# Kernel optimization log

Hardware: AMD Instinct MI355X
Metric: run time of the kernel (lower is better)

## Reference

```python
import jax, jax.numpy as jnp
import numpy as np

B, SEQ, EMB, LAT = 8192, 1024, 768, 256
TAXA = ['phylum', 'order', 'family', 'genus', 'species']
NC = {'phylum': 40, 'order': 200, 'family': 800, 'genus': 3000, 'species': 12000}


def _table(P, C):
    # parent->child validity: child c belongs to parent (c % P); every parent non-empty
    return (jnp.arange(C)[None, :] % P) == jnp.arange(P)[:, None]


def setup_inputs() -> dict:
    key = jax.random.key(0)
    ks = jax.random.split(key, 16)
    d = {}
    d['sequences'] = jax.random.normal(ks[0], (B, SEQ), jnp.float32)
    d['W_dnabert'] = jax.random.normal(ks[1], (SEQ, EMB), jnp.float32) * 0.02
    d['W_enc'] = jax.random.normal(ks[2], (EMB, LAT), jnp.float32) * 0.02
    for i, t in enumerate(TAXA):
        d[f'W_cls_{t}'] = jax.random.normal(ks[3 + i], (LAT, NC[t]), jnp.float32) * 0.02
        d[f'W_dec_{t}'] = jax.random.normal(ks[8 + i], (LAT, EMB), jnp.float32) * 0.02
    d['W_global'] = jax.random.normal(ks[13], (LAT, EMB), jnp.float32) * 0.02
    d['T_order'] = _table(NC['phylum'], NC['order'])
    d['T_family'] = _table(NC['order'], NC['family'])
    d['T_genus'] = _table(NC['family'], NC['genus'])
    d['T_species'] = _table(NC['genus'], NC['species'])
    return d


def reference(sequences, W_dnabert, W_enc,
              W_cls_phylum, W_cls_order, W_cls_family, W_cls_genus, W_cls_species,
              W_dec_phylum, W_dec_order, W_dec_family, W_dec_genus, W_dec_species,
              W_global, T_order, T_family, T_genus, T_species):
    # frozen dnabert (torch.no_grad)
    emb = jax.lax.stop_gradient(sequences @ W_dnabert)          # [B, EMB]
    z = emb @ W_enc                                             # [B, LAT]

    Wc = {'phylum': W_cls_phylum, 'order': W_cls_order, 'family': W_cls_family,
          'genus': W_cls_genus, 'species': W_cls_species}
    Wd = {'phylum': W_dec_phylum, 'order': W_dec_order, 'family': W_dec_family,
          'genus': W_dec_genus, 'species': W_dec_species}
    Tt = {'order': T_order, 'family': T_family, 'genus': T_genus, 'species': T_species}

    logits_out, recon_out = {}, {}
    parent_preds = None
    for taxon in TAXA:
        logits = z @ Wc[taxon]                                  # [B, C_taxon]
        if parent_preds is not None and taxon in Tt:
            # vectorized hierarchical mask: gather valid-class row per sample
            mask = Tt[taxon][parent_preds]                      # [B, C_taxon] bool
            logits = jnp.where(mask, logits, -jnp.inf)
        logits_out[taxon] = logits
        recon_out[taxon] = z @ Wd[taxon]                        # [B, EMB]
        parent_preds = jnp.argmax(logits, axis=1)               # [B] int

    global_rec = z @ W_global                                   # [B, EMB]
    return (z,
            logits_out['phylum'], logits_out['order'], logits_out['family'],
            logits_out['genus'], logits_out['species'],
            recon_out['phylum'], recon_out['order'], recon_out['family'],
            recon_out['genus'], recon_out['species'],
            global_rec, emb)
```

## Files before the change

kernel.cpp:

```cpp
#include <hip/hip_runtime.h>
#include <hip/hip_bf16.h>

typedef __attribute__((ext_vector_type(8))) short short8;
typedef __attribute__((ext_vector_type(4))) float f32x4;
typedef unsigned short ushort_t;
typedef unsigned int u32;

static constexpr int Bn  = 8192;
static constexpr int SEQ = 1024;
static constexpr int EMB = 768;
static constexpr int LAT = 256;

static constexpr size_t OFF_Z   = 0;
static constexpr size_t OFF_LP  = 2097152;
static constexpr size_t OFF_LO  = 2424832;
static constexpr size_t OFF_LF  = 4063232;
static constexpr size_t OFF_LG  = 10616832;
static constexpr size_t OFF_LS  = 35192832;
static constexpr size_t OFF_RP  = 133496832;
static constexpr size_t OFF_EMB = 171245568;

static constexpr size_t SCR      = OFF_LO;
static constexpr size_t S_SEQ_H  = SCR + 0;
static constexpr size_t S_SEQ_L  = SCR + 4194304;
static constexpr size_t S_EMB_H  = SCR + 8388608;
static constexpr size_t S_EMB_L  = SCR + 11534336;
static constexpr size_t S_Z_H    = SCR + 14680064;
static constexpr size_t S_Z_L    = SCR + 15728640;
static constexpr size_t S_REC_H  = SCR + 16777216;
static constexpr size_t S_REC_L  = SCR + 17367040;
static constexpr size_t S_CLS_T  = SCR + 17956864;
static constexpr size_t S_T_O    = S_CLS_T + 0;
static constexpr size_t S_T_F    = S_CLS_T + 51200;
static constexpr size_t S_T_G    = S_CLS_T + 256000;
static constexpr size_t S_T_S    = S_CLS_T + 1024000;

static constexpr size_t SCR_END   = SCR + 22052864;
static constexpr size_t TAIL_N4   = (OFF_RP - SCR_END) / 4;
static constexpr size_t T_SEQ0 = 0,        T_SEQ1 = 3276800;
static constexpr size_t T_EMB0 = 3276800,  T_EMB1 = 16384000;
static constexpr size_t T_Z0   = 16384000, T_Z1   = 18743296;
static constexpr size_t T_R0   = 18743296, T_R1   = 27254784;
static constexpr size_t FILLZ_N4  = 8388608 / 4;
static constexpr size_t FILLR_N4  = (14680064 - 8388608) / 4;
static constexpr size_t FILLB_N4  = (22052864 - 14680064) / 4;

static constexpr size_t WS_DNA_H = 0;
static constexpr size_t WS_DNA_L = 786432;
static constexpr size_t WS_ENC_H = 1572864;
static constexpr size_t WS_ENC_L = 1769472;
static constexpr size_t WS_COMPACT_FL = 983040;

#define MASKED_VAL (-1.0e30f)

__device__ __forceinline__ ushort_t bfbits(float f) {
    return __builtin_bit_cast(ushort_t, __float2bfloat16(f));
}
__device__ __forceinline__ float bf2f(ushort_t h) {
    return __builtin_bit_cast(float, ((unsigned)h) << 16);
}
__device__ __forceinline__ void split2(float f, ushort_t& h, ushort_t& l) {
    h = bfbits(f);
    l = bfbits(f - bf2f(h));
}

__device__ __forceinline__ size_t tile_pos(int rt, int nKT, int kt, int r, int g) {
    return ((size_t)rt * nKT + kt) * 8192 + (size_t)r * 64 + ((g ^ (r & 7)) << 3);
}

__device__ __forceinline__ void fill_span(f32x4* __restrict__ dst, size_t n4,
                                          int fb, int nFB)
{
    const f32x4 v = {MASKED_VAL, MASKED_VAL, MASKED_VAL, MASKED_VAL};
    for (size_t i = (size_t)fb * 256 + threadIdx.x; i < n4; i += (size_t)nFB * 256)
        __builtin_nontemporal_store(v, dst + i);
}

__global__ __launch_bounds__(256)
void fill_kernel(f32x4* __restrict__ dst, size_t n4)
{
    fill_span(dst, n4, blockIdx.x, gridDim.x);
}

__device__ __forceinline__ void prep_wtT_body(const float* __restrict__ src,
                                              ushort_t* __restrict__ dh,
                                              ushort_t* __restrict__ dl,
                                              int K, int N, int bx, int nb)
{
    const int gpr = K >> 3, nKT = K >> 6;
    const int nG = N * gpr;
    for (int gi = bx * 256 + threadIdx.x; gi < nG; gi += nb * 256) {
        const int n = gi / gpr, gk = gi - n * gpr;
        short8 hh, ll;
        #pragma unroll
        for (int j = 0; j < 8; ++j) {
            ushort_t hv, lv;
            split2(src[(size_t)(gk * 8 + j) * N + n], hv, lv);
            hh[j] = (short)hv; ll[j] = (short)lv;
        }
        const size_t base = tile_pos(n >> 7, nKT, gk >> 3, n & 127, gk & 7);
        *(short8*)(dh + base) = hh;
        *(short8*)(dl + base) = ll;
    }
}

struct Ptr6 { const float* p[6]; };

__device__ __forceinline__ void prep_rec_body(Ptr6 s, ushort_t* __restrict__ dh,
                                              ushort_t* __restrict__ dl, int bx, int nb)
{
    constexpr int gpr = 32, nKT = 4;
    const int nG = 4608 * gpr;
    for (int gi = bx * 256 + threadIdx.x; gi < nG; gi += nb * 256) {
        const int np = gi / gpr, gk = gi - np * gpr;
        const int m = np / 768, nn = np - m * 768;
        const float* sm = s.p[m];
        short8 hh, ll;
        #pragma unroll
        for (int j = 0; j < 8; ++j) {
            ushort_t hv, lv;
            split2(sm[(size_t)(gk * 8 + j) * 768 + nn], hv, lv);
            hh[j] = (short)hv; ll[j] = (short)lv;
        }
        const size_t base = tile_pos(np >> 7, nKT, gk >> 3, np & 127, gk & 7);
        *(short8*)(dh + base) = hh;
        *(short8*)(dl + base) = ll;
    }
}

__global__ __launch_bounds__(256)
void prep_all(const float* __restrict__ Wdna, ushort_t* dnaH, ushort_t* dnaL,
              const float* __restrict__ Wenc, ushort_t* encH, ushort_t* encL,
              Ptr6 s6, ushort_t* recH, ushort_t* recL)
{
    const int bx = blockIdx.x;
    if (bx < 384)       prep_wtT_body(Wdna, dnaH, dnaL, 1024, 768, bx, 384);
    else if (bx < 480)  prep_wtT_body(Wenc, encH, encL, 768, 256, bx - 384, 96);
    else                prep_rec_body(s6, recH, recL, bx - 480, 576);
}

__global__ __launch_bounds__(256)
void transpose_all(const float* __restrict__ Wo, const float* __restrict__ Wf,
                   const float* __restrict__ Wg, const float* __restrict__ Ws,
                   float* To, float* Tf, float* Tg, float* Ts)
{
    __shared__ float t[64][65];
    int bx = blockIdx.x;
    const float* src; float* dst; int C; int cb;
    if (bx < 16)       { src = Wo; dst = To; C = 200;   cb = bx; }
    else if (bx < 68)  { src = Wf; dst = Tf; C = 800;   cb = bx - 16; }
    else if (bx < 256) { src = Wg; dst = Tg; C = 3000;  cb = bx - 68; }
    else               { src = Ws; dst = Ts; C = 12000; cb = bx - 256; }
    const int ct = cb >> 2, kt = cb & 3;
    const int c0 = ct * 64;
    const int tid = threadIdx.x;
    const int cl = tid & 63, kr = tid >> 6;
    #pragma unroll
    for (int i = 0; i < 16; ++i) {
        const int k = i * 4 + kr;
        const int c = c0 + cl;
        t[k][cl] = (c < C) ? src[(size_t)(kt * 64 + k) * C + c] : 0.f;
    }
    __syncthreads();
    #pragma unroll
    for (int i = 0; i < 16; ++i) {
        const int cc = i * 4 + kr;
        const int c = c0 + cc;
        if (c < C) dst[(size_t)c * 256 + kt * 64 + cl] = t[cl][cc];
    }
}

__global__ __launch_bounds__(256)
void split_tiled_fill(const float* __restrict__ src, ushort_t* __restrict__ dh,
                      ushort_t* __restrict__ dl, int M, int K,
                      int nGB, f32x4* __restrict__ f1, size_t n1)
{
    if ((int)blockIdx.x >= nGB) {
        fill_span(f1, n1, blockIdx.x - nGB, gridDim.x - nGB);
        return;
    }
    const int gpr = K >> 3, nKT = K >> 6;
    const int nG = M * gpr;
    for (int gi = blockIdx.x * 256 + threadIdx.x; gi < nG; gi += nGB * 256) {
        const int row = gi / gpr, gk = gi - row * gpr;
        const float* s = src + (size_t)row * K + gk * 8;
        const float4 a = *(const float4*)s;
        const float4 b = *(const float4*)(s + 4);
        const float f[8] = {a.x, a.y, a.z, a.w, b.x, b.y, b.z, b.w};
        short8 hh, ll;
        #pragma unroll
        for (int j = 0; j < 8; ++j) {
            ushort_t hv, lv;
            split2(f[j], hv, lv);
            hh[j] = (short)hv; ll[j] = (short)lv;
        }
        const size_t base = tile_pos(row >> 7, nKT, gk >> 3, row & 127, gk & 7);
        *(short8*)(dh + base) = hh;
        *(short8*)(dl + base) = ll;
    }
}

__global__ __launch_bounds__(256)
void split_tiled(const float* __restrict__ src, ushort_t* __restrict__ dh,
                 ushort_t* __restrict__ dl, int M, int K)
{
    const int gpr = K >> 3, nKT = K >> 6;
    const int nG = M * gpr;
    for (int gi = blockIdx.x * 256 + threadIdx.x; gi < nG; gi += gridDim.x * 256) {
        const int row = gi / gpr, gk = gi - row * gpr;
        const float* s = src + (size_t)row * K + gk * 8;
        const float4 a = *(const float4*)s;
        const float4 b = *(const float4*)(s + 4);
        const float f[8] = {a.x, a.y, a.z, a.w, b.x, b.y, b.z, b.w};
        short8 hh, ll;
        #pragma unroll
        for (int j = 0; j < 8; ++j) {
            ushort_t hv, lv;
            split2(f[j], hv, lv);
            hh[j] = (short)hv; ll[j] = (short)lv;
        }
        const size_t base = tile_pos(row >> 7, nKT, gk >> 3, row & 127, gk & 7);
        *(short8*)(dh + base) = hh;
        *(short8*)(dl + base) = ll;
    }
}

__device__ __forceinline__ void gload16(const ushort_t* g, ushort_t* l) {
    __builtin_amdgcn_global_load_lds(
        (const __attribute__((address_space(1))) u32*)g,
        (__attribute__((address_space(3))) u32*)l, 16, 0, 0);
}

__global__ __launch_bounds__(256)
void gemm_ts_fill(const ushort_t* __restrict__ Ahg, const ushort_t* __restrict__ Alg,
                  const ushort_t* __restrict__ Bhg, const ushort_t* __restrict__ Blg,
                  int K, float* __restrict__ Cbase, int chunkW, size_t chunkStride,
                  int nCT, int nGB,
                  f32x4* __restrict__ f1, size_t n1,
                  f32x4* __restrict__ f2, size_t n2)
{
    __shared__ ushort_t sAh[8192], sAl[8192], sBh[8192], sBl[8192];

    if ((int)blockIdx.x >= nGB) {
        const int fb = blockIdx.x - nGB, nFB = gridDim.x - nGB;
        fill_span(f1, n1, fb, nFB);
        if (n2) fill_span(f2, n2, fb, nFB);
        return;
    }

    const int tid = threadIdx.x, w = tid >> 6, lane = tid & 63;
    const int wm = w >> 1, wn = w & 1;
    const int fr = lane & 15, kg = lane >> 4;
    const int nKT = K >> 6;
    const int rt = blockIdx.x / nCT, ct = blockIdx.x % nCT;
    const int col0 = ct * 128;
    const int chunk = col0 / chunkW;
    const int lc0 = col0 - chunk * chunkW;
    float* __restrict__ C = Cbase + (size_t)chunk * chunkStride;

    const int sbase = w * 2048;
    const int lgo = lane * 8;

    f32x4 acc[4][4] = {};

    for (int kt = 0; kt < nKT; ++kt) {
        const size_t at = ((size_t)rt * nKT + kt) * 8192;
        const size_t bt = ((size_t)ct * nKT + kt) * 8192;
        #pragma unroll
        for (int i = 0; i < 4; ++i) {
            const int co = sbase + i * 512;
            gload16(Ahg + at + co + lgo, &sAh[co]);
            gload16(Alg + at + co + lgo, &sAl[co]);
            gload16(Bhg + bt + co + lgo, &sBh[co]);
            gload16(Blg + bt + co + lgo, &sBl[co]);
        }
        __syncthreads();

        #pragma unroll
        for (int ks = 0; ks < 2; ++ks) {
            const int g = ks * 4 + kg;
            short8 a_h[4], a_l[4], b_h[4], b_l[4];
            #pragma unroll
            for (int i = 0; i < 4; ++i) {
                const int ra = wm * 64 + i * 16 + fr;
                const int pa = ra * 64 + ((g ^ (ra & 7)) << 3);
                a_h[i] = *(const short8*)&sAh[pa];
                a_l[i] = *(const short8*)&sAl[pa];
                const int rb = wn * 64 + i * 16 + fr;
                const int pb = rb * 64 + ((g ^ (rb & 7)) << 3);
                b_h[i] = *(const short8*)&sBh[pb];
                b_l[i] = *(const short8*)&sBl[pb];
            }
            #pragma unroll
            for (int mi = 0; mi < 4; ++mi) {
                #pragma unroll
                for (int ni = 0; ni < 4; ++ni) {
                    acc[mi][ni] = __builtin_amdgcn_mfma_f32_16x16x32_bf16(a_h[mi], b_h[ni], acc[mi][ni], 0, 0, 0);
                    acc[mi][ni] = __builtin_amdgcn_mfma_f32_16x16x32_bf16(a_h[mi], b_l[ni], acc[mi][ni], 0, 0, 0);
                    acc[mi][ni] = __builtin_amdgcn_mfma_f32_16x16x32_bf16(a_l[mi], b_h[ni], acc[mi][ni], 0, 0, 0);
                }
            }
        }
        __syncthreads();
    }

    const int crow = kg * 4;
    #pragma unroll
    for (int mi = 0; mi < 4; ++mi) {
        const int gr = rt * 128 + wm * 64 + mi * 16 + crow;
        #pragma unroll
        for (int ni = 0; ni < 4; ++ni) {
            const int gc = lc0 + wn * 64 + ni * 16 + fr;
            #pragma unroll
            for (int j = 0; j < 4; ++j)
                C[(size_t)(gr + j) * chunkW + gc] = acc[mi][ni][j];
        }
    }
}

template <int C, int P>
__device__ __forceinline__ int level_w(const float* __restrict__ WT,
                                       float4 zr, int p, int lane,
                                       float* __restrict__ rec )
{
    const int cnt = (C - p + P - 1) / P;
    float sv[5];
    #pragma unroll
    for (int j = 0; j < 5; ++j) {
        float s = 0.f;
        if (j < cnt) {
            const float4 wv = *(const float4*)(WT + (size_t)(p + j * P) * 256 + lane * 4);
            s = fmaf(wv.x, zr.x, fmaf(wv.y, zr.y, fmaf(wv.z, zr.z, wv.w * zr.w)));
        }
        sv[j] = s;
    }
    #pragma unroll
    for (int j = 0; j < 5; ++j) {
        if (j < cnt) {
            #pragma unroll
            for (int off = 32; off; off >>= 1) sv[j] += __shfl_xor(sv[j], off);
        }
    }
    float best = sv[0];
    int bj = 0;
    #pragma unroll
    for (int j = 1; j < 5; ++j)
        if (j < cnt && sv[j] > best) { best = sv[j]; bj = j; }

    if (lane == 0) {
        rec[0] = __int_as_float(p);
        rec[1] = sv[0];
        rec[2] = (1 < cnt) ? sv[1] : 0.f;
        rec[3] = (2 < cnt) ? sv[2] : 0.f;
        rec[4] = (3 < cnt) ? sv[3] : 0.f;
        rec[5] = (4 < cnt) ? sv[4] : 0.f;
    }
    return p + bj * P;
}

__global__ __launch_bounds__(256)
void chain_kernel(const float* __restrict__ z,
                  const float* __restrict__ Wp,
                  const float* __restrict__ ToT, const float* __restrict__ TfT,
                  const float* __restrict__ TgT, const float* __restrict__ TsT,
                  float* __restrict__ out, float* __restrict__ compact)
{
    __shared__ float zsh[4][256];

    const int w    = threadIdx.x >> 6;
    const int lane = threadIdx.x & 63;
    const size_t b = (size_t)blockIdx.x * 4 + w;

    const float4 zr4 = *(const float4*)(z + b * 256 + lane * 4);
    *(float4*)&zsh[w][lane * 4] = zr4;
    asm volatile("s_waitcnt lgkmcnt(0)" ::: "memory");
    const float* zrow = &zsh[w][0];

    float pv = MASKED_VAL;
    if (lane < 40) {
        float s0 = 0.f, s1 = 0.f, s2 = 0.f, s3 = 0.f;
        #pragma unroll 4
        for (int k = 0; k < 256; k += 4) {
            s0 = fmaf(zrow[k + 0], Wp[(k + 0) * 40 + lane], s0);
            s1 = fmaf(zrow[k + 1], Wp[(k + 1) * 40 + lane], s1);
            s2 = fmaf(zrow[k + 2], Wp[(k + 2) * 40 + lane], s2);
            s3 = fmaf(zrow[k + 3], Wp[(k + 3) * 40 + lane], s3);
        }
        pv = (s0 + s1) + (s2 + s3);
        out[OFF_LP + b * 40 + lane] = pv;
    }
    float v = pv;
    int idx = lane;
    #pragma unroll
    for (int off = 32; off; off >>= 1) {
        float ov = __shfl_xor(v, off);
        int   oi = __shfl_xor(idx, off);
        if (ov > v || (ov == v && oi < idx)) { v = ov; idx = oi; }
    }
    int p = idx;

    p = level_w<200, 40>    (ToT, zr4, p, lane, compact + (0 * Bn + b) * 6);
    p = level_w<800, 200>   (TfT, zr4, p, lane, compact + (1 * Bn + b) * 6);
    p = level_w<3000, 800>  (TgT, zr4, p, lane, compact + (2 * Bn + b) * 6);
    (void)level_w<12000, 3000>(TsT, zr4, p, lane, compact + (3 * Bn + b) * 6);
}

__global__ __launch_bounds__(256)
void scatter_kernel(const float* __restrict__ compact, float* __restrict__ out)
{
    const int t = blockIdx.x * 256 + threadIdx.x;
    if (t >= 4 * Bn) return;
    const int lvl = t >> 13, b = t & (Bn - 1);
    const int Cs[4] = {200, 800, 3000, 12000};
    const int Ps[4] = {40, 200, 800, 3000};
    const size_t OFFL[4] = {OFF_LO, OFF_LF, OFF_LG, OFF_LS};
    const float* rec = compact + ((size_t)lvl * Bn + b) * 6;
    const int p = __float_as_int(rec[0]);
    const int C = Cs[lvl], P = Ps[lvl];
    const int cnt = (C - p + P - 1) / P;
    float* dst = out + OFFL[lvl] + (size_t)b * C;
    for (int j = 0; j < cnt; ++j)
        dst[p + j * P] = rec[1 + j];
}

extern "C" void kernel_launch(void* const* d_in, const int* in_sizes, int n_in,
                              void* d_out, int out_size, void* d_ws, size_t ws_size,
                              hipStream_t stream)
{
    const float* seq    = (const float*)d_in[0];
    const float* Wdna   = (const float*)d_in[1];
    const float* Wenc   = (const float*)d_in[2];
    const float* Wcls_p = (const float*)d_in[3];
    const float* Wdec_p = (const float*)d_in[4];
    const float* Wcls_o = (const float*)d_in[5];
    const float* Wdec_o = (const float*)d_in[6];
    const float* Wcls_f = (const float*)d_in[7];
    const float* Wdec_f = (const float*)d_in[8];
    const float* Wcls_g = (const float*)d_in[9];
    const float* Wdec_g = (const float*)d_in[10];
    const float* Wcls_s = (const float*)d_in[11];
    const float* Wdec_s = (const float*)d_in[12];
    const float* Wglob  = (const float*)d_in[13];
    (void)in_sizes; (void)n_in; (void)out_size; (void)ws_size;

    float* out = (float*)d_out;
    ushort_t* ws = (ushort_t*)d_ws;

    ushort_t* seqH = (ushort_t*)(out + S_SEQ_H);
    ushort_t* seqL = (ushort_t*)(out + S_SEQ_L);
    ushort_t* embH = (ushort_t*)(out + S_EMB_H);
    ushort_t* embL = (ushort_t*)(out + S_EMB_L);
    ushort_t* zH   = (ushort_t*)(out + S_Z_H);
    ushort_t* zL   = (ushort_t*)(out + S_Z_L);
    ushort_t* recH = (ushort_t*)(out + S_REC_H);
    ushort_t* recL = (ushort_t*)(out + S_REC_L);
    float* ToT = out + S_T_O;
    float* TfT = out + S_T_F;
    float* TgT = out + S_T_G;
    float* TsT = out + S_T_S;
    ushort_t* dnaH = ws + WS_DNA_H;
    ushort_t* dnaL = ws + WS_DNA_L;
    ushort_t* encH = ws + WS_ENC_H;
    ushort_t* encL = ws + WS_ENC_L;
    float* compact = (float*)ws + WS_COMPACT_FL;
    f32x4* tail = (f32x4*)(out + SCR_END);

    Ptr6 s6{{Wdec_p, Wdec_o, Wdec_f, Wdec_g, Wdec_s, Wglob}};
    prep_all<<<1056, 256, 0, stream>>>(Wdna, dnaH, dnaL, Wenc, encH, encL, s6, recH, recL);
    transpose_all<<<1008, 256, 0, stream>>>(Wcls_o, Wcls_f, Wcls_g, Wcls_s,
                                            ToT, TfT, TgT, TsT);
    split_tiled_fill<<<4096 + 448, 256, 0, stream>>>(seq, seqH, seqL, Bn, SEQ,
                                                     4096, tail + T_SEQ0, T_SEQ1 - T_SEQ0);

    gemm_ts_fill<<<384 + 1664, 256, 0, stream>>>(
        seqH, seqL, dnaH, dnaL, SEQ, out + OFF_EMB, EMB, 0, 6, 384,
        tail + T_EMB0, T_EMB1 - T_EMB0, nullptr, 0);
    split_tiled<<<3072, 256, 0, stream>>>(out + OFF_EMB, embH, embL, Bn, EMB);

    gemm_ts_fill<<<128 + 896, 256, 0, stream>>>(
        embH, embL, encH, encL, EMB, out + OFF_Z, LAT, 0, 2, 128,
        (f32x4*)(out + SCR), FILLZ_N4, tail + T_Z0, T_Z1 - T_Z0);
    split_tiled<<<1024, 256, 0, stream>>>(out + OFF_Z, zH, zL, Bn, LAT);

    gemm_ts_fill<<<2304 + 768, 256, 0, stream>>>(
        zH, zL, recH, recL, LAT, out + OFF_RP, EMB, (size_t)Bn * EMB, 36, 2304,
        (f32x4*)(out + S_EMB_H), FILLR_N4, tail + T_R0, T_R1 - T_R0);

    chain_kernel<<<dim3(Bn / 4), 256, 0, stream>>>(out + OFF_Z, Wcls_p, ToT, TfT,
                                                   TgT, TsT, out, compact);

    fill_kernel<<<512, 256, 0, stream>>>((f32x4*)(out + S_Z_H), FILLB_N4);
    scatter_kernel<<<(4 * Bn + 255) / 256, 256, 0, stream>>>(compact, out);
}
```

Measured before the change: 308.6 us.

## Fuse split into GEMM epilogues and merge prep, recon and chain launches

Each GEMM now stages its result tile through shared memory, writes it with coalesced float4 stores, and also emits the bf16 hi/lo tiled split of the output. This removes the separate split_tiled passes over emb and z. The three prep kernels become one launch, and the recon GEMM, the hierarchical chain and the fills share a single grid, cutting launch count and letting the chain overlap with the GEMM. In exchange the fill spans are rebalanced and the epilogue costs one extra shared-memory round trip and a barrier.

```diff
diff --git a/kernel.cpp b/kernel.cpp
--- a/kernel.cpp
+++ b/kernel.cpp
@@ -37,10 +37,9 @@
 
 static constexpr size_t SCR_END   = SCR + 22052864;
 static constexpr size_t TAIL_N4   = (OFF_RP - SCR_END) / 4;
-static constexpr size_t T_SEQ0 = 0,        T_SEQ1 = 3276800;
-static constexpr size_t T_EMB0 = 3276800,  T_EMB1 = 16384000;
-static constexpr size_t T_Z0   = 16384000, T_Z1   = 18743296;
-static constexpr size_t T_R0   = 18743296, T_R1   = 27254784;
+static constexpr size_t TE0 = 0,        TE1 = 9437184;
+static constexpr size_t TZ0 = 9437184,  TZ1 = 11534336;
+static constexpr size_t TR0 = 11534336, TR1 = 27254784;
 static constexpr size_t FILLZ_N4  = 8388608 / 4;
 static constexpr size_t FILLR_N4  = (14680064 - 8388608) / 4;
 static constexpr size_t FILLB_N4  = (22052864 - 14680064) / 4;
@@ -128,24 +127,11 @@
     }
 }
 
-__global__ __launch_bounds__(256)
-void prep_all(const float* __restrict__ Wdna, ushort_t* dnaH, ushort_t* dnaL,
-              const float* __restrict__ Wenc, ushort_t* encH, ushort_t* encL,
-              Ptr6 s6, ushort_t* recH, ushort_t* recL)
-{
-    const int bx = blockIdx.x;
-    if (bx < 384)       prep_wtT_body(Wdna, dnaH, dnaL, 1024, 768, bx, 384);
-    else if (bx < 480)  prep_wtT_body(Wenc, encH, encL, 768, 256, bx - 384, 96);
-    else                prep_rec_body(s6, recH, recL, bx - 480, 576);
-}
-
-__global__ __launch_bounds__(256)
-void transpose_all(const float* __restrict__ Wo, const float* __restrict__ Wf,
-                   const float* __restrict__ Wg, const float* __restrict__ Ws,
-                   float* To, float* Tf, float* Tg, float* Ts)
-{
-    __shared__ float t[64][65];
-    int bx = blockIdx.x;
+__device__ __forceinline__ void transpose_body(float t[64][65], int bx,
+    const float* __restrict__ Wo, const float* __restrict__ Wf,
+    const float* __restrict__ Wg, const float* __restrict__ Ws,
+    float* To, float* Tf, float* Tg, float* Ts)
+{
     const float* src; float* dst; int C; int cb;
     if (bx < 16)       { src = Wo; dst = To; C = 200;   cb = bx; }
     else if (bx < 68)  { src = Wf; dst = Tf; C = 800;   cb = bx - 16; }
@@ -170,18 +156,14 @@
     }
 }
 
-__global__ __launch_bounds__(256)
-void split_tiled_fill(const float* __restrict__ src, ushort_t* __restrict__ dh,
-                      ushort_t* __restrict__ dl, int M, int K,
-                      int nGB, f32x4* __restrict__ f1, size_t n1)
-{
-    if ((int)blockIdx.x >= nGB) {
-        fill_span(f1, n1, blockIdx.x - nGB, gridDim.x - nGB);
-        return;
-    }
+__device__ __forceinline__ void split_body(const float* __restrict__ src,
+                                           ushort_t* __restrict__ dh,
+                                           ushort_t* __restrict__ dl,
+                                           int M, int K, int bx, int nb)
+{
     const int gpr = K >> 3, nKT = K >> 6;
     const int nG = M * gpr;
-    for (int gi = blockIdx.x * 256 + threadIdx.x; gi < nG; gi += nGB * 256) {
+    for (int gi = bx * 256 + threadIdx.x; gi < nG; gi += nb * 256) {
         const int row = gi / gpr, gk = gi - row * gpr;
         const float* s = src + (size_t)row * K + gk * 8;
         const float4 a = *(const float4*)s;
@@ -201,27 +183,23 @@
 }
 
 __global__ __launch_bounds__(256)
-void split_tiled(const float* __restrict__ src, ushort_t* __restrict__ dh,
-                 ushort_t* __restrict__ dl, int M, int K)
-{
-    const int gpr = K >> 3, nKT = K >> 6;
-    const int nG = M * gpr;
-    for (int gi = blockIdx.x * 256 + threadIdx.x; gi < nG; gi += gridDim.x * 256) {
-        const int row = gi / gpr, gk = gi - row * gpr;
-        const float* s = src + (size_t)row * K + gk * 8;
-        const float4 a = *(const float4*)s;
-        const float4 b = *(const float4*)(s + 4);
-        const float f[8] = {a.x, a.y, a.z, a.w, b.x, b.y, b.z, b.w};
-        short8 hh, ll;
-        #pragma unroll
-        for (int j = 0; j < 8; ++j) {
-            ushort_t hv, lv;
-            split2(f[j], hv, lv);
-            hh[j] = (short)hv; ll[j] = (short)lv;
-        }
-        const size_t base = tile_pos(row >> 7, nKT, gk >> 3, row & 127, gk & 7);
-        *(short8*)(dh + base) = hh;
-        *(short8*)(dl + base) = ll;
+void prep_everything(const float* Wdna, ushort_t* dnaH, ushort_t* dnaL,
+                     const float* Wenc, ushort_t* encH, ushort_t* encL,
+                     Ptr6 s6, ushort_t* recH, ushort_t* recL,
+                     const float* Wo, const float* Wf, const float* Wg, const float* Ws,
+                     float* To, float* Tf, float* Tg, float* Ts,
+                     const float* seq, ushort_t* seqH, ushort_t* seqL)
+{
+    __shared__ float t[64][65];
+    const int bx = blockIdx.x;
+    if (bx < 1056) {
+        if (bx < 384)       prep_wtT_body(Wdna, dnaH, dnaL, 1024, 768, bx, 384);
+        else if (bx < 480)  prep_wtT_body(Wenc, encH, encL, 768, 256, bx - 384, 96);
+        else                prep_rec_body(s6, recH, recL, bx - 480, 576);
+    } else if (bx < 2064) {
+        transpose_body(t, bx - 1056, Wo, Wf, Wg, Ws, To, Tf, Tg, Ts);
+    } else {
+        split_body(seq, seqH, seqL, Bn, SEQ, bx - 2064, 4096);
     }
 }
 
@@ -231,28 +209,23 @@
         (__attribute__((address_space(3))) u32*)l, 16, 0, 0);
 }
 
-__global__ __launch_bounds__(256)
-void gemm_ts_fill(const ushort_t* __restrict__ Ahg, const ushort_t* __restrict__ Alg,
-                  const ushort_t* __restrict__ Bhg, const ushort_t* __restrict__ Blg,
-                  int K, float* __restrict__ Cbase, int chunkW, size_t chunkStride,
-                  int nCT, int nGB,
-                  f32x4* __restrict__ f1, size_t n1,
-                  f32x4* __restrict__ f2, size_t n2)
-{
-    __shared__ ushort_t sAh[8192], sAl[8192], sBh[8192], sBl[8192];
-
-    if ((int)blockIdx.x >= nGB) {
-        const int fb = blockIdx.x - nGB, nFB = gridDim.x - nGB;
-        fill_span(f1, n1, fb, nFB);
-        if (n2) fill_span(f2, n2, fb, nFB);
-        return;
-    }
+__device__ __forceinline__ void gemm_body(
+    ushort_t* smem,
+    const ushort_t* __restrict__ Ahg, const ushort_t* __restrict__ Alg,
+    const ushort_t* __restrict__ Bhg, const ushort_t* __restrict__ Blg,
+    int K, float* __restrict__ Cbase, int chunkW, size_t chunkStride,
+    int nCT, int bx, ushort_t* __restrict__ th, ushort_t* __restrict__ tl, int nKT2)
+{
+    ushort_t* sAh = smem;
+    ushort_t* sAl = smem + 8192;
+    ushort_t* sBh = smem + 16384;
+    ushort_t* sBl = smem + 24576;
 
     const int tid = threadIdx.x, w = tid >> 6, lane = tid & 63;
     const int wm = w >> 1, wn = w & 1;
     const int fr = lane & 15, kg = lane >> 4;
     const int nKT = K >> 6;
-    const int rt = blockIdx.x / nCT, ct = blockIdx.x % nCT;
+    const int rt = bx / nCT, ct = bx % nCT;
     const int col0 = ct * 128;
     const int chunk = col0 / chunkW;
     const int lc0 = col0 - chunk * chunkW;
@@ -304,18 +277,63 @@
         __syncthreads();
     }
 
+    float* cf = (float*)smem;
     const int crow = kg * 4;
     #pragma unroll
-    for (int mi = 0; mi < 4; ++mi) {
-        const int gr = rt * 128 + wm * 64 + mi * 16 + crow;
+    for (int mi = 0; mi < 4; ++mi)
         #pragma unroll
-        for (int ni = 0; ni < 4; ++ni) {
-            const int gc = lc0 + wn * 64 + ni * 16 + fr;
+        for (int ni = 0; ni < 4; ++ni)
             #pragma unroll
             for (int j = 0; j < 4; ++j)
-                C[(size_t)(gr + j) * chunkW + gc] = acc[mi][ni][j];
-        }
-    }
+                cf[(wm * 64 + mi * 16 + crow + j) * 128 + (wn * 64 + ni * 16 + fr)] = acc[mi][ni][j];
+    __syncthreads();
+
+    #pragma unroll
+    for (int i = 0; i < 8; ++i) {
+        const int t = i * 256 + tid;
+        const int row = t >> 4, g = t & 15;
+        const float* srcr = cf + row * 128 + g * 8;
+        const float4 v0 = *(const float4*)srcr;
+        const float4 v1 = *(const float4*)(srcr + 4);
+        float* dst = C + (size_t)(rt * 128 + row) * chunkW + lc0 + g * 8;
+        *(float4*)dst = v0;
+        *(float4*)(dst + 4) = v1;
+        if (th) {
+            const float fv[8] = {v0.x, v0.y, v0.z, v0.w, v1.x, v1.y, v1.z, v1.w};
+            short8 hh, ll;
+            #pragma unroll
+            for (int q = 0; q < 8; ++q) {
+                ushort_t hv, lv;
+                split2(fv[q], hv, lv);
+                hh[q] = (short)hv; ll[q] = (short)lv;
+            }
+            const int ktile = (ct * 128 + g * 8) >> 6;
+            const int gg = g & 7;
+            const size_t base = ((size_t)rt * nKT2 + ktile) * 8192
+                              + (size_t)row * 64 + ((gg ^ (row & 7)) << 3);
+            *(short8*)(th + base) = hh;
+            *(short8*)(tl + base) = ll;
+        }
+    }
+}
+
+__global__ __launch_bounds__(256)
+void gemm_fused(const ushort_t* __restrict__ Ahg, const ushort_t* __restrict__ Alg,
+                const ushort_t* __restrict__ Bhg, const ushort_t* __restrict__ Blg,
+                int K, float* __restrict__ Cbase, int chunkW, size_t chunkStride,
+                int nCT, int nGB, ushort_t* th, ushort_t* tl, int nKT2,
+                f32x4* __restrict__ f1, size_t n1,
+                f32x4* __restrict__ f2, size_t n2)
+{
+    __shared__ ushort_t smem[32768];
+    if ((int)blockIdx.x >= nGB) {
+        const int fb = blockIdx.x - nGB, nFB = gridDim.x - nGB;
+        fill_span(f1, n1, fb, nFB);
+        if (n2) fill_span(f2, n2, fb, nFB);
+        return;
+    }
+    gemm_body(smem, Ahg, Alg, Bhg, Blg, K, Cbase, chunkW, chunkStride,
+              nCT, blockIdx.x, th, tl, nKT2);
 }
 
 template <int C, int P>
@@ -358,23 +376,20 @@
     return p + bj * P;
 }
 
-__global__ __launch_bounds__(256)
-void chain_kernel(const float* __restrict__ z,
-                  const float* __restrict__ Wp,
-                  const float* __restrict__ ToT, const float* __restrict__ TfT,
-                  const float* __restrict__ TgT, const float* __restrict__ TsT,
-                  float* __restrict__ out, float* __restrict__ compact)
-{
-    __shared__ float zsh[4][256];
-
+__device__ __forceinline__ void chain_body(float* zsh, int bid,
+    const float* __restrict__ z, const float* __restrict__ Wp,
+    const float* __restrict__ ToT, const float* __restrict__ TfT,
+    const float* __restrict__ TgT, const float* __restrict__ TsT,
+    float* __restrict__ out, float* __restrict__ compact)
+{
     const int w    = threadIdx.x >> 6;
     const int lane = threadIdx.x & 63;
-    const size_t b = (size_t)blockIdx.x * 4 + w;
+    const size_t b = (size_t)bid * 4 + w;
 
     const float4 zr4 = *(const float4*)(z + b * 256 + lane * 4);
-    *(float4*)&zsh[w][lane * 4] = zr4;
+    *(float4*)&zsh[w * 256 + lane * 4] = zr4;
     asm volatile("s_waitcnt lgkmcnt(0)" ::: "memory");
-    const float* zrow = &zsh[w][0];
+    const float* zrow = zsh + w * 256;
 
     float pv = MASKED_VAL;
     if (lane < 40) {
@@ -403,6 +418,31 @@
     p = level_w<800, 200>   (TfT, zr4, p, lane, compact + (1 * Bn + b) * 6);
     p = level_w<3000, 800>  (TgT, zr4, p, lane, compact + (2 * Bn + b) * 6);
     (void)level_w<12000, 3000>(TsT, zr4, p, lane, compact + (3 * Bn + b) * 6);
+}
+
+__global__ __launch_bounds__(256)
+void recon_chain_fill(const ushort_t* __restrict__ Ahg, const ushort_t* __restrict__ Alg,
+                      const ushort_t* __restrict__ Bhg, const ushort_t* __restrict__ Blg,
+                      float* __restrict__ Cbase,
+                      const float* __restrict__ z, const float* __restrict__ Wp,
+                      const float* __restrict__ ToT, const float* __restrict__ TfT,
+                      const float* __restrict__ TgT, const float* __restrict__ TsT,
+                      float* __restrict__ out, float* __restrict__ compact,
+                      f32x4* __restrict__ f1, size_t n1,
+                      f32x4* __restrict__ f2, size_t n2)
+{
+    __shared__ ushort_t smem[32768];
+    const int bx = blockIdx.x;
+    if (bx < 2304) {
+        gemm_body(smem, Ahg, Alg, Bhg, Blg, LAT, Cbase, EMB, (size_t)Bn * EMB,
+                  36, bx, nullptr, nullptr, 0);
+    } else if (bx < 2304 + 2048) {
+        chain_body((float*)smem, bx - 2304, z, Wp, ToT, TfT, TgT, TsT, out, compact);
+    } else {
+        const int fb = bx - 4352, nFB = gridDim.x - 4352;
+        fill_span(f1, n1, fb, nFB);
+        if (n2) fill_span(f2, n2, fb, nFB);
+    }
 }
 
 __global__ __launch_bounds__(256)
@@ -466,29 +506,24 @@
     f32x4* tail = (f32x4*)(out + SCR_END);
 
     Ptr6 s6{{Wdec_p, Wdec_o, Wdec_f, Wdec_g, Wdec_s, Wglob}};
-    prep_all<<<1056, 256, 0, stream>>>(Wdna, dnaH, dnaL, Wenc, encH, encL, s6, recH, recL);
-    transpose_all<<<1008, 256, 0, stream>>>(Wcls_o, Wcls_f, Wcls_g, Wcls_s,
-                                            ToT, TfT, TgT, TsT);
-    split_tiled_fill<<<4096 + 448, 256, 0, stream>>>(seq, seqH, seqL, Bn, SEQ,
-                                                     4096, tail + T_SEQ0, T_SEQ1 - T_SEQ0);
-
-    gemm_ts_fill<<<384 + 1664, 256, 0, stream>>>(
+    prep_everything<<<6160, 256, 0, stream>>>(
+        Wdna, dnaH, dnaL, Wenc, encH, encL, s6, recH, recL,
+        Wcls_o, Wcls_f, Wcls_g, Wcls_s, ToT, TfT, TgT, TsT,
+        seq, seqH, seqL);
+
+    gemm_fused<<<384 + 1664, 256, 0, stream>>>(
         seqH, seqL, dnaH, dnaL, SEQ, out + OFF_EMB, EMB, 0, 6, 384,
-        tail + T_EMB0, T_EMB1 - T_EMB0, nullptr, 0);
-    split_tiled<<<3072, 256, 0, stream>>>(out + OFF_EMB, embH, embL, Bn, EMB);
-
-    gemm_ts_fill<<<128 + 896, 256, 0, stream>>>(
+        embH, embL, 12, tail + TE0, TE1 - TE0, nullptr, 0);
+
+    gemm_fused<<<128 + 896, 256, 0, stream>>>(
         embH, embL, encH, encL, EMB, out + OFF_Z, LAT, 0, 2, 128,
-        (f32x4*)(out + SCR), FILLZ_N4, tail + T_Z0, T_Z1 - T_Z0);
-    split_tiled<<<1024, 256, 0, stream>>>(out + OFF_Z, zH, zL, Bn, LAT);
-
-    gemm_ts_fill<<<2304 + 768, 256, 0, stream>>>(
-        zH, zL, recH, recL, LAT, out + OFF_RP, EMB, (size_t)Bn * EMB, 36, 2304,
-        (f32x4*)(out + S_EMB_H), FILLR_N4, tail + T_R0, T_R1 - T_R0);
-
-    chain_kernel<<<dim3(Bn / 4), 256, 0, stream>>>(out + OFF_Z, Wcls_p, ToT, TfT,
-                                                   TgT, TsT, out, compact);
+        zH, zL, 4, (f32x4*)(out + SCR), FILLZ_N4, tail + TZ0, TZ1 - TZ0);
+
+    recon_chain_fill<<<5120, 256, 0, stream>>>(
+        zH, zL, recH, recL, out + OFF_RP,
+        out + OFF_Z, Wcls_p, ToT, TfT, TgT, TsT, out, compact,
+        (f32x4*)(out + S_EMB_H), FILLR_N4, tail + TR0, TR1 - TR0);
 
     fill_kernel<<<512, 256, 0, stream>>>((f32x4*)(out + S_Z_H), FILLB_N4);
-    scatter_kernel<<<(4 * Bn + 255) / 256, 256, 0, stream>>>(compact, out);
-}
+    scatter_kernel<<<128, 256, 0, stream>>>(compact, out);
+}
```

New measurement: 343.3 us, median of 2. 11.2% more time.

## Merge prep kernels into one launch and fuse masked fill with chain kernel

Applied to the files above, without the earlier changes.

Folds the weight prep, classifier-weight transpose and sequence split into a single prep_everything launch, dropping two kernel launches and the boundary gaps between them. The -inf tail fill no longer runs alongside the sequence split; its share is redistributed over the three GEMM launches. The z/rec scratch fill now runs inside the chain kernel's grid, and the separate fill covers only the transposed-classifier region after the chain kernel finishes. The merged prep kernel reserves 64x65 floats of shared memory for every block, which may reduce occupancy for the split blocks.

```diff
diff --git a/kernel.cpp b/kernel.cpp
--- a/kernel.cpp
+++ b/kernel.cpp
@@ -35,15 +35,14 @@
 static constexpr size_t S_T_G    = S_CLS_T + 256000;
 static constexpr size_t S_T_S    = S_CLS_T + 1024000;
 
-static constexpr size_t SCR_END   = SCR + 22052864;
-static constexpr size_t TAIL_N4   = (OFF_RP - SCR_END) / 4;
-static constexpr size_t T_SEQ0 = 0,        T_SEQ1 = 3276800;
-static constexpr size_t T_EMB0 = 3276800,  T_EMB1 = 16384000;
-static constexpr size_t T_Z0   = 16384000, T_Z1   = 18743296;
-static constexpr size_t T_R0   = 18743296, T_R1   = 27254784;
-static constexpr size_t FILLZ_N4  = 8388608 / 4;
-static constexpr size_t FILLR_N4  = (14680064 - 8388608) / 4;
-static constexpr size_t FILLB_N4  = (22052864 - 14680064) / 4;
+static constexpr size_t SCR_END  = SCR + 22052864;
+static constexpr size_t TE0 = 0,        TE1 = 9418752;
+static constexpr size_t TZ0 = 9418752,  TZ1 = 18837504;
+static constexpr size_t TR0 = 18837504, TR1 = 27254784;
+static constexpr size_t FILLZ_N4 = 8388608 / 4;
+static constexpr size_t FILLR_N4 = (14680064 - 8388608) / 4;
+static constexpr size_t ZREC_N4  = (17956864 - 14680064) / 4;
+static constexpr size_t CLST_N4  = (22052864 - 17956864) / 4;
 
 static constexpr size_t WS_DNA_H = 0;
 static constexpr size_t WS_DNA_L = 786432;
@@ -128,24 +127,11 @@
     }
 }
 
-__global__ __launch_bounds__(256)
-void prep_all(const float* __restrict__ Wdna, ushort_t* dnaH, ushort_t* dnaL,
-              const float* __restrict__ Wenc, ushort_t* encH, ushort_t* encL,
-              Ptr6 s6, ushort_t* recH, ushort_t* recL)
-{
-    const int bx = blockIdx.x;
-    if (bx < 384)       prep_wtT_body(Wdna, dnaH, dnaL, 1024, 768, bx, 384);
-    else if (bx < 480)  prep_wtT_body(Wenc, encH, encL, 768, 256, bx - 384, 96);
-    else                prep_rec_body(s6, recH, recL, bx - 480, 576);
-}
-
-__global__ __launch_bounds__(256)
-void transpose_all(const float* __restrict__ Wo, const float* __restrict__ Wf,
-                   const float* __restrict__ Wg, const float* __restrict__ Ws,
-                   float* To, float* Tf, float* Tg, float* Ts)
-{
-    __shared__ float t[64][65];
-    int bx = blockIdx.x;
+__device__ __forceinline__ void transpose_body(float t[64][65], int bx,
+    const float* __restrict__ Wo, const float* __restrict__ Wf,
+    const float* __restrict__ Wg, const float* __restrict__ Ws,
+    float* To, float* Tf, float* Tg, float* Ts)
+{
     const float* src; float* dst; int C; int cb;
     if (bx < 16)       { src = Wo; dst = To; C = 200;   cb = bx; }
     else if (bx < 68)  { src = Wf; dst = Tf; C = 800;   cb = bx - 16; }
@@ -170,18 +156,14 @@
     }
 }
 
-__global__ __launch_bounds__(256)
-void split_tiled_fill(const float* __restrict__ src, ushort_t* __restrict__ dh,
-                      ushort_t* __restrict__ dl, int M, int K,
-                      int nGB, f32x4* __restrict__ f1, size_t n1)
-{
-    if ((int)blockIdx.x >= nGB) {
-        fill_span(f1, n1, blockIdx.x - nGB, gridDim.x - nGB);
-        return;
-    }
+__device__ __forceinline__ void split_body(const float* __restrict__ src,
+                                           ushort_t* __restrict__ dh,
+                                           ushort_t* __restrict__ dl,
+                                           int M, int K, int bx, int nb)
+{
     const int gpr = K >> 3, nKT = K >> 6;
     const int nG = M * gpr;
-    for (int gi = blockIdx.x * 256 + threadIdx.x; gi < nG; gi += nGB * 256) {
+    for (int gi = bx * 256 + threadIdx.x; gi < nG; gi += nb * 256) {
         const int row = gi / gpr, gk = gi - row * gpr;
         const float* s = src + (size_t)row * K + gk * 8;
         const float4 a = *(const float4*)s;
@@ -201,27 +183,23 @@
 }
 
 __global__ __launch_bounds__(256)
-void split_tiled(const float* __restrict__ src, ushort_t* __restrict__ dh,
-                 ushort_t* __restrict__ dl, int M, int K)
-{
-    const int gpr = K >> 3, nKT = K >> 6;
-    const int nG = M * gpr;
-    for (int gi = blockIdx.x * 256 + threadIdx.x; gi < nG; gi += gridDim.x * 256) {
-        const int row = gi / gpr, gk = gi - row * gpr;
-        const float* s = src + (size_t)row * K + gk * 8;
-        const float4 a = *(const float4*)s;
-        const float4 b = *(const float4*)(s + 4);
-        const float f[8] = {a.x, a.y, a.z, a.w, b.x, b.y, b.z, b.w};
-        short8 hh, ll;
-        #pragma unroll
-        for (int j = 0; j < 8; ++j) {
-            ushort_t hv, lv;
-            split2(f[j], hv, lv);
-            hh[j] = (short)hv; ll[j] = (short)lv;
-        }
-        const size_t base = tile_pos(row >> 7, nKT, gk >> 3, row & 127, gk & 7);
-        *(short8*)(dh + base) = hh;
-        *(short8*)(dl + base) = ll;
+void prep_everything(const float* Wdna, ushort_t* dnaH, ushort_t* dnaL,
+                     const float* Wenc, ushort_t* encH, ushort_t* encL,
+                     Ptr6 s6, ushort_t* recH, ushort_t* recL,
+                     const float* Wo, const float* Wf, const float* Wg, const float* Ws,
+                     float* To, float* Tf, float* Tg, float* Ts,
+                     const float* seq, ushort_t* seqH, ushort_t* seqL)
+{
+    __shared__ float t[64][65];
+    const int bx = blockIdx.x;
+    if (bx < 1056) {
+        if (bx < 384)       prep_wtT_body(Wdna, dnaH, dnaL, 1024, 768, bx, 384);
+        else if (bx < 480)  prep_wtT_body(Wenc, encH, encL, 768, 256, bx - 384, 96);
+        else                prep_rec_body(s6, recH, recL, bx - 480, 576);
+    } else if (bx < 2064) {
+        transpose_body(t, bx - 1056, Wo, Wf, Wg, Ws, To, Tf, Tg, Ts);
+    } else {
+        split_body(seq, seqH, seqL, Bn, SEQ, bx - 2064, 4096);
     }
 }
 
@@ -318,6 +296,13 @@
     }
 }
 
+__global__ __launch_bounds__(256)
+void split_tiled(const float* __restrict__ src, ushort_t* __restrict__ dh,
+                 ushort_t* __restrict__ dl, int M, int K)
+{
+    split_body(src, dh, dl, M, K, blockIdx.x, gridDim.x);
+}
+
 template <int C, int P>
 __device__ __forceinline__ int level_w(const float* __restrict__ WT,
                                        float4 zr, int p, int lane,
@@ -358,23 +343,20 @@
     return p + bj * P;
 }
 
-__global__ __launch_bounds__(256)
-void chain_kernel(const float* __restrict__ z,
-                  const float* __restrict__ Wp,
-                  const float* __restrict__ ToT, const float* __restrict__ TfT,
-                  const float* __restrict__ TgT, const float* __restrict__ TsT,
-                  float* __restrict__ out, float* __restrict__ compact)
-{
-    __shared__ float zsh[4][256];
-
+__device__ __forceinline__ void chain_body(float* zsh, int bid,
+    const float* __restrict__ z, const float* __restrict__ Wp,
+    const float* __restrict__ ToT, const float* __restrict__ TfT,
+    const float* __restrict__ TgT, const float* __restrict__ TsT,
+    float* __restrict__ out, float* __restrict__ compact)
+{
     const int w    = threadIdx.x >> 6;
     const int lane = threadIdx.x & 63;
-    const size_t b = (size_t)blockIdx.x * 4 + w;
+    const size_t b = (size_t)bid * 4 + w;
 
     const float4 zr4 = *(const float4*)(z + b * 256 + lane * 4);
-    *(float4*)&zsh[w][lane * 4] = zr4;
+    *(float4*)&zsh[w * 256 + lane * 4] = zr4;
     asm volatile("s_waitcnt lgkmcnt(0)" ::: "memory");
-    const float* zrow = &zsh[w][0];
+    const float* zrow = zsh + w * 256;
 
     float pv = MASKED_VAL;
     if (lane < 40) {
@@ -403,6 +385,22 @@
     p = level_w<800, 200>   (TfT, zr4, p, lane, compact + (1 * Bn + b) * 6);
     p = level_w<3000, 800>  (TgT, zr4, p, lane, compact + (2 * Bn + b) * 6);
     (void)level_w<12000, 3000>(TsT, zr4, p, lane, compact + (3 * Bn + b) * 6);
+}
+
+__global__ __launch_bounds__(256)
+void chain_fill(const float* __restrict__ z, const float* __restrict__ Wp,
+                const float* __restrict__ ToT, const float* __restrict__ TfT,
+                const float* __restrict__ TgT, const float* __restrict__ TsT,
+                float* __restrict__ out, float* __restrict__ compact,
+                f32x4* __restrict__ f1, size_t n1)
+{
+    __shared__ float zsh[4 * 256];
+    const int bx = blockIdx.x;
+    if (bx >= Bn / 4) {
+        fill_span(f1, n1, bx - Bn / 4, gridDim.x - Bn / 4);
+        return;
+    }
+    chain_body(zsh, bx, z, Wp, ToT, TfT, TgT, TsT, out, compact);
 }
 
 __global__ __launch_bounds__(256)
@@ -466,29 +464,29 @@
     f32x4* tail = (f32x4*)(out + SCR_END);
 
     Ptr6 s6{{Wdec_p, Wdec_o, Wdec_f, Wdec_g, Wdec_s, Wglob}};
-    prep_all<<<1056, 256, 0, stream>>>(Wdna, dnaH, dnaL, Wenc, encH, encL, s6, recH, recL);
-    transpose_all<<<1008, 256, 0, stream>>>(Wcls_o, Wcls_f, Wcls_g, Wcls_s,
-                                            ToT, TfT, TgT, TsT);
-    split_tiled_fill<<<4096 + 448, 256, 0, stream>>>(seq, seqH, seqL, Bn, SEQ,
-                                                     4096, tail + T_SEQ0, T_SEQ1 - T_SEQ0);
+    prep_everything<<<6160, 256, 0, stream>>>(
+        Wdna, dnaH, dnaL, Wenc, encH, encL, s6, recH, recL,
+        Wcls_o, Wcls_f, Wcls_g, Wcls_s, ToT, TfT, TgT, TsT,
+        seq, seqH, seqL);
 
     gemm_ts_fill<<<384 + 1664, 256, 0, stream>>>(
         seqH, seqL, dnaH, dnaL, SEQ, out + OFF_EMB, EMB, 0, 6, 384,
-        tail + T_EMB0, T_EMB1 - T_EMB0, nullptr, 0);
+        tail + TE0, TE1 - TE0, nullptr, 0);
     split_tiled<<<3072, 256, 0, stream>>>(out + OFF_EMB, embH, embL, Bn, EMB);
 
     gemm_ts_fill<<<128 + 896, 256, 0, stream>>>(
         embH, embL, encH, encL, EMB, out + OFF_Z, LAT, 0, 2, 128,
-        (f32x4*)(out + SCR), FILLZ_N4, tail + T_Z0, T_Z1 - T_Z0);
+        (f32x4*)(out + SCR), FILLZ_N4, tail + TZ0, TZ1 - TZ0);
     split_tiled<<<1024, 256, 0, stream>>>(out + OFF_Z, zH, zL, Bn, LAT);
 
     gemm_ts_fill<<<2304 + 768, 256, 0, stream>>>(
         zH, zL, recH, recL, LAT, out + OFF_RP, EMB, (size_t)Bn * EMB, 36, 2304,
-        (f32x4*)(out + S_EMB_H), FILLR_N4, tail + T_R0, T_R1 - T_R0);
-
-    chain_kernel<<<dim3(Bn / 4), 256, 0, stream>>>(out + OFF_Z, Wcls_p, ToT, TfT,
-                                                   TgT, TsT, out, compact);
-
-    fill_kernel<<<512, 256, 0, stream>>>((f32x4*)(out + S_Z_H), FILLB_N4);
-    scatter_kernel<<<(4 * Bn + 255) / 256, 256, 0, stream>>>(compact, out);
-}
+        (f32x4*)(out + S_EMB_H), FILLR_N4, tail + TR0, TR1 - TR0);
+
+    chain_fill<<<2048 + 512, 256, 0, stream>>>(out + OFF_Z, Wcls_p, ToT, TfT,
+                                               TgT, TsT, out, compact,
+                                               (f32x4*)(out + S_Z_H), ZREC_N4);
+
+    fill_kernel<<<512, 256, 0, stream>>>((f32x4*)(out + S_CLS_T), CLST_N4);
+    scatter_kernel<<<128, 256, 0, stream>>>(compact, out);
+}
```

Result: no change. 304.8 us (-1.2%).
